# Kernel optimization log

Measured on AMD Instinct MI355X. Metric: run time of the kernel, lower is better.

## Reference

```python
import jax, jax.numpy as jnp
import numpy as np

B, T, C, H, W = 16, 5, 512, 16, 16
NUM_FEAT = 10
K_IN = T * H * W          # 1280, conv1/G3 in_channels
G_OUT = NUM_FEAT * H * W  # 2560, G3 out_channels


def setup_inputs() -> dict:
    key = jax.random.key(0)
    ks = jax.random.split(key, 9)
    inp = {
        "input": jax.random.normal(ks[0], (B, T, C, H, W), dtype=jnp.float32),
        "input1": jax.random.normal(ks[1], (B, T, C, H, W), dtype=jnp.float32),
        "act_weights": jax.random.uniform(ks[2], (3,), dtype=jnp.float32),
        # Conv1d kernels with kernel_size=1 stored as [out_ch, in_ch]
        "conv1_w": jax.random.normal(ks[3], (NUM_FEAT, K_IN), dtype=jnp.float32) / np.sqrt(K_IN),
        "conv1_b": jax.random.normal(ks[4], (NUM_FEAT,), dtype=jnp.float32) * 0.01,
        "G3_w": jax.random.normal(ks[5], (G_OUT, K_IN), dtype=jnp.float32) / np.sqrt(K_IN),
        "G3_b": jax.random.normal(ks[6], (G_OUT,), dtype=jnp.float32) * 0.01,
        "ffnn1_w": jax.random.normal(ks[7], (C, C), dtype=jnp.float32) / np.sqrt(C),
        "ffnn1_b": jax.random.normal(ks[8], (C,), dtype=jnp.float32) * 0.01,
    }
    return inp


def reference(input, input1, act_weights, conv1_w, conv1_b, G3_w, G3_b, ffnn1_w, ffnn1_b):
    b, t, c, h, w = input.shape
    nf = conv1_w.shape[0]
    # [B,T,C,H,W] -> [B,C,T*H*W] -> transpose to [B, T*H*W, C] (conv1d channel axis = T*H*W)
    x = jnp.transpose(input, (0, 2, 1, 3, 4)).reshape(b, c, t * h * w)
    x = jnp.swapaxes(x, 1, 2)  # [B, K_IN, C]

    # conv1 (1x1 conv == GEMM over channel axis): [B, nf, C]
    c1 = jnp.einsum("fk,bkc->bfc", conv1_w, x) + conv1_b[None, :, None]
    # transpose -> [B, C, nf]; AvgPool1d(nf) -> mean over nf -> [B, C]
    pooled = jnp.mean(jnp.swapaxes(c1, 1, 2), axis=-1)
    # shared linear (same ffnn1 used in all three branches)
    pre = pooled @ ffnn1_w.T + ffnn1_b  # [B, C]

    # G3: [B, G_OUT, C] -> permute -> [B, C, G_OUT]
    g3 = jnp.einsum("gk,bkc->bgc", G3_w, x) + G3_b[None, :, None]
    g3 = jnp.swapaxes(g3, 1, 2)  # [B, C, G_OUT]

    # diag_embed(v) @ M == v[..., None] * M  -> fuse the three branches into one scale
    scale = (act_weights[0] * jax.nn.relu(pre)
             + act_weights[1] * jax.nn.sigmoid(pre)
             + act_weights[2] * jax.nn.softmax(pre, axis=1))  # [B, C]

    out = scale[:, :, None] * g3  # [B, C, nf*H*W]
    out = out.reshape(b, c, nf, h, w)
    return jnp.transpose(out, (0, 2, 1, 3, 4))  # [B, nf, C, H, W]
```

## Files before the change

### kernel.cpp

```cpp
#include <hip/hip_runtime.h>
#include <hip/hip_bf16.h>
#include <stdint.h>

#define B_   16
#define T_   5
#define C_   512
#define HW_  256
#define NF_  10
#define KIN_ 1280
#define GOUT_ 2560

typedef __attribute__((ext_vector_type(8))) short s16x8;
typedef __attribute__((ext_vector_type(4))) float f32x4;
typedef unsigned short u16;

__device__ __forceinline__ u16 f2bf(float x) {
    unsigned int u = __float_as_uint(x);
    return (u16)((u + 0x7FFFu + ((u >> 16) & 1u)) >> 16);
}

#define CASTW_N8  (GOUT_ * KIN_ / 8)
#define CASTW_BLKS (CASTW_N8 / 256)

__global__ __launch_bounds__(256) void k_init(const float* __restrict__ conv1_w,
                        const float* __restrict__ conv1_b,
                        float* __restrict__ wbar, float* __restrict__ bbar,
                        const float* __restrict__ g3w,
                        u16* __restrict__ wsA) {
    if (blockIdx.x < 5) {
        int k = blockIdx.x * 256 + threadIdx.x;
        float s = 0.f;
        #pragma unroll
        for (int f = 0; f < NF_; ++f) s += conv1_w[f * KIN_ + k];
        wbar[k] = s * (1.0f / NF_);
        if (blockIdx.x == 0 && threadIdx.x == 0) {
            float sb = 0.f;
            #pragma unroll
            for (int f = 0; f < NF_; ++f) sb += conv1_b[f];
            *bbar = sb * (1.0f / NF_);
        }
        return;
    }
    int i = (blockIdx.x - 5) * 256 + threadIdx.x;
    if (i < CASTW_N8) {
        const float4* s = reinterpret_cast<const float4*>(g3w) + (size_t)i * 2;
        float4 v0 = s[0], v1 = s[1];
        union { u16 h[8]; int4 v; } u;
        u.h[0] = f2bf(v0.x); u.h[1] = f2bf(v0.y); u.h[2] = f2bf(v0.z); u.h[3] = f2bf(v0.w);
        u.h[4] = f2bf(v1.x); u.h[5] = f2bf(v1.y); u.h[6] = f2bf(v1.z); u.h[7] = f2bf(v1.w);
        reinterpret_cast<int4*>(wsA)[i] = u.v;
    }
}

__global__ void k_wbar(const float* __restrict__ conv1_w,
                       const float* __restrict__ conv1_b,
                       float* __restrict__ wbar, float* __restrict__ bbar) {
    int k = blockIdx.x * blockDim.x + threadIdx.x;
    if (k < KIN_) {
        float s = 0.f;
        #pragma unroll
        for (int f = 0; f < NF_; ++f) s += conv1_w[f * KIN_ + k];
        wbar[k] = s * (1.0f / NF_);
    }
    if (blockIdx.x == 0 && threadIdx.x == 0) {
        float s = 0.f;
        #pragma unroll
        for (int f = 0; f < NF_; ++f) s += conv1_b[f];
        *bbar = s * (1.0f / NF_);
    }
}

#define FUSE_BLKS (B_ * C_)

__global__ __launch_bounds__(256) void k_prep(const float* __restrict__ in,
                         const float* __restrict__ wbar,
                         const float* __restrict__ bbar,
                         float* __restrict__ pooled,
                         u16* __restrict__ X) {
    int bc = blockIdx.x;
    int b = bc >> 9;
    int c = bc & 511;
    int tid = threadIdx.x;

    float s = 0.f;
    if (tid < 160) {
        int t   = tid >> 5;
        int hw0 = (tid & 31) * 8;
        size_t off = ((size_t)(b * T_ + t) * C_ + c) * HW_ + hw0;
        const float4* ip = reinterpret_cast<const float4*>(in + off);
        float4 v0 = ip[0], v1 = ip[1];
        const float4* wp = reinterpret_cast<const float4*>(wbar + t * HW_ + hw0);
        float4 w0 = wp[0], w1 = wp[1];
        s = v0.x * w0.x + v0.y * w0.y + v0.z * w0.z + v0.w * w0.w
          + v1.x * w1.x + v1.y * w1.y + v1.z * w1.z + v1.w * w1.w;
        union { u16 h[8]; int4 q; } u;
        u.h[0] = f2bf(v0.x); u.h[1] = f2bf(v0.y); u.h[2] = f2bf(v0.z); u.h[3] = f2bf(v0.w);
        u.h[4] = f2bf(v1.x); u.h[5] = f2bf(v1.y); u.h[6] = f2bf(v1.z); u.h[7] = f2bf(v1.w);
        reinterpret_cast<int4*>(X + off)[0] = u.q;
    }

    #pragma unroll
    for (int off = 32; off > 0; off >>= 1) s += __shfl_down(s, off, 64);
    __shared__ float red[4];
    int wid = tid >> 6, lane = tid & 63;
    if (lane == 0) red[wid] = s;
    __syncthreads();
    if (tid == 0) {
        float tot = red[0] + red[1] + red[2] + red[3];
        pooled[bc] = tot + *bbar;
    }
}

__global__ __launch_bounds__(256) void k_pooled(const float* __restrict__ in,
                         const float* __restrict__ wbar,
                         const float* __restrict__ bbar,
                         float* __restrict__ pooled) {
    int bc = blockIdx.x;
    int b = bc >> 9;
    int c = bc & 511;
    int hw = threadIdx.x;
    const float* base = in + ((size_t)(b * T_) * C_ + c) * HW_;
    float s = 0.f;
    #pragma unroll
    for (int t = 0; t < T_; ++t)
        s = fmaf(wbar[t * HW_ + hw], base[(size_t)t * C_ * HW_ + hw], s);
    #pragma unroll
    for (int off = 32; off > 0; off >>= 1) s += __shfl_down(s, off, 64);
    __shared__ float red[4];
    int wid = threadIdx.x >> 6, lane = threadIdx.x & 63;
    if (lane == 0) red[wid] = s;
    __syncthreads();
    if (threadIdx.x == 0) {
        float tot = red[0] + red[1] + red[2] + red[3];
        pooled[bc] = tot + *bbar;
    }
}

__global__ __launch_bounds__(256) void k_pre(const float* __restrict__ pooled,
                       const float* __restrict__ ffnn1_w,
                       const float* __restrict__ ffnn1_b,
                       float* __restrict__ pre) {
    int b   = blockIdx.x >> 4;
    int grp = blockIdx.x & 15;
    int wid = threadIdx.x >> 6, lane = threadIdx.x & 63;

    const float4* pp = reinterpret_cast<const float4*>(pooled + b * C_ + lane * 8);
    float4 pa = pp[0], pb = pp[1];

    #pragma unroll
    for (int rr = 0; rr < 8; ++rr) {
        int c = grp * 32 + wid * 8 + rr;
        const float4* wr = reinterpret_cast<const float4*>(ffnn1_w + (size_t)c * C_ + lane * 8);
        float4 wa = wr[0], wb2 = wr[1];
        float d = pa.x * wa.x + pa.y * wa.y + pa.z * wa.z + pa.w * wa.w
                + pb.x * wb2.x + pb.y * wb2.y + pb.z * wb2.z + pb.w * wb2.w;
        #pragma unroll
        for (int off = 32; off > 0; off >>= 1) d += __shfl_xor(d, off, 64);
        if (lane == 0) pre[b * C_ + c] = d + ffnn1_b[c];
    }
}

__global__ __launch_bounds__(512) void k_act(const float* __restrict__ pre,
                       const float* __restrict__ actw,
                       float* __restrict__ scale) {
    int b = blockIdx.x;
    int tid = threadIdx.x;
    int wid = tid >> 6, lane = tid & 63;
    __shared__ float redm[8], reds[8];

    float p0 = pre[b * C_ + tid];
    float mx = p0;
    #pragma unroll
    for (int off = 32; off > 0; off >>= 1) mx = fmaxf(mx, __shfl_xor(mx, off, 64));
    if (lane == 0) redm[wid] = mx;
    __syncthreads();
    float m8 = redm[0];
    #pragma unroll
    for (int i = 1; i < 8; ++i) m8 = fmaxf(m8, redm[i]);
    float e0 = __expf(p0 - m8);
    float sm = e0;
    #pragma unroll
    for (int off = 32; off > 0; off >>= 1) sm += __shfl_xor(sm, off, 64);
    if (lane == 0) reds[wid] = sm;
    __syncthreads();
    float ssum = reds[0];
    #pragma unroll
    for (int i = 1; i < 8; ++i) ssum += reds[i];

    float aw0 = actw[0], aw1 = actw[1], aw2 = actw[2];
    scale[b * C_ + tid] = aw0 * fmaxf(p0, 0.f)
                        + aw1 * (1.f / (1.f + __expf(-p0)))
                        + aw2 * (e0 / ssum);
}

__global__ __launch_bounds__(512) void k_scale(const float* __restrict__ pooled,
                        const float* __restrict__ ffnn1_w,
                        const float* __restrict__ ffnn1_b,
                        const float* __restrict__ actw,
                        float* __restrict__ scale) {
    int b = blockIdx.x;
    int c = threadIdx.x;
    __shared__ float sp[C_];
    __shared__ float red[8];

    sp[c] = pooled[b * C_ + c];
    __syncthreads();

    float acc = ffnn1_b[c];
    const float* wr = ffnn1_w + (size_t)c * C_;
    #pragma unroll 8
    for (int j = 0; j < C_; ++j) acc = fmaf(wr[j], sp[j], acc);

    int wid = c >> 6, lane = c & 63;
    float m = acc;
    #pragma unroll
    for (int off = 32; off > 0; off >>= 1) m = fmaxf(m, __shfl_down(m, off, 64));
    if (lane == 0) red[wid] = m;
    __syncthreads();
    if (c == 0) {
        float mm = red[0];
        #pragma unroll
        for (int i = 1; i < 8; ++i) mm = fmaxf(mm, red[i]);
        red[0] = mm;
    }
    __syncthreads();
    m = red[0];
    __syncthreads();

    float e = __expf(acc - m);
    float s = e;
    #pragma unroll
    for (int off = 32; off > 0; off >>= 1) s += __shfl_down(s, off, 64);
    if (lane == 0) red[wid] = s;
    __syncthreads();
    if (c == 0) {
        float ss = 0.f;
        #pragma unroll
        for (int i = 0; i < 8; ++i) ss += red[i];
        red[0] = ss;
    }
    __syncthreads();
    s = red[0];

    float w0 = actw[0], w1 = actw[1], w2 = actw[2];
    float val = w0 * fmaxf(acc, 0.f)
              + w1 * (1.f / (1.f + __expf(-acc)))
              + w2 * (e / s);
    scale[b * C_ + c] = val;
}

#define BM 160
#define BN 256
#define BK 32
#define NKT (KIN_ / BK)
#define ABUF (BM * BK)
#define BBUF (BN * BK)
#define BUFU (ABUF + BBUF)

__device__ __forceinline__ void gload16(const void* g, void* l) {
    __builtin_amdgcn_global_load_lds(
        (const __attribute__((address_space(1))) void*)g,
        (__attribute__((address_space(3))) void*)l, 16, 0, 0);
}

__global__ __launch_bounds__(256, 2) void k_gemm_mfma(
    const u16* __restrict__ A,
    const u16* __restrict__ X,
    const float* __restrict__ g3b,
    const float* __restrict__ scale,
    float* __restrict__ out)
{
    __shared__ u16 lds[2 * BUFU];

    int orig = blockIdx.x;
    int xcd  = orig & 7;
    int idx  = orig >> 3;
    int nt   = xcd * 4 + (idx >> 4);
    int gt   = idx & 15;
    int g0   = gt * BM;
    int b    = nt >> 1;
    int c0   = (nt & 1) * BN;

    int tid = threadIdx.x;
    int lane = tid & 63, wid = tid >> 6;
    int lrow = lane & 15, lslot = lane >> 4;

    int offA0, offA1, offA2, offB0, offB1, offB2, offB3;
    {
        int q, r, p;
        q = tid;        r = q >> 2; p = q & 3; offA0 = r * KIN_ + (p ^ ((r >> 1) & 3)) * 8;
        q = 256 + tid;  r = q >> 2; p = q & 3; offA1 = r * KIN_ + (p ^ ((r >> 1) & 3)) * 8;
        q = 512 + tid;  r = q >> 2; p = q & 3; offA2 = r * KIN_ + (p ^ ((r >> 1) & 3)) * 8;
        q = tid;        r = q >> 2; p = q & 3; offB0 = r * HW_  + (p ^ ((r >> 1) & 3)) * 8;
        q = 256 + tid;  r = q >> 2; p = q & 3; offB1 = r * HW_  + (p ^ ((r >> 1) & 3)) * 8;
        q = 512 + tid;  r = q >> 2; p = q & 3; offB2 = r * HW_  + (p ^ ((r >> 1) & 3)) * 8;
        q = 768 + tid;  r = q >> 2; p = q & 3; offB3 = r * HW_  + (p ^ ((r >> 1) & 3)) * 8;
    }
    int wb = wid * 512;

    const u16* Abase = A + (size_t)g0 * KIN_;
    #define XOFF(kt) ((((size_t)(b * T_ + ((kt) >> 3)) * C_) + c0) * HW_ + ((kt) & 7) * 32)

    #define STAGE(D, sA, sX)                                                 \
    {                                                                        \
        gload16((sA) + offA0, (D) + wb);                                     \
        gload16((sA) + offA1, (D) + 2048 + wb);                              \
        if (tid < 128) gload16((sA) + offA2, (D) + 4096 + wb);               \
        gload16((sX) + offB0, (D) + ABUF + wb);                              \
        gload16((sX) + offB1, (D) + ABUF + 2048 + wb);                       \
        gload16((sX) + offB2, (D) + ABUF + 4096 + wb);                       \
        gload16((sX) + offB3, (D) + ABUF + 6144 + wb);                       \
    }

    STAGE(lds, Abase, X + XOFF(0));
    __syncthreads();

    f32x4 acc[10][4];
    #pragma unroll
    for (int m = 0; m < 10; ++m)
        #pragma unroll
        for (int n = 0; n < 4; ++n) acc[m][n] = (f32x4)0.f;

    int cur = 0;
    for (int t = 0; t < NKT; ++t) {
        const u16* Ac = lds + cur * BUFU;
        const u16* Bc = Ac + ABUF;
        if (t + 1 < NKT) {
            u16* Dn = lds + (cur ^ 1) * BUFU;
            const u16* sA = Abase + (size_t)(t + 1) * BK;
            const u16* sX = X + XOFF(t + 1);
            STAGE(Dn, sA, sX);
        }

        s16x8 b0[4];
        #pragma unroll
        for (int n = 0; n < 4; ++n) {
            int r = wid * 64 + n * 16 + lrow;
            int p = lslot ^ ((r >> 1) & 3);
            b0[n] = *reinterpret_cast<const s16x8*>(Bc + r * BK + p * 8);
        }
        __builtin_amdgcn_s_setprio(1);
        #pragma unroll
        for (int m = 0; m < 10; ++m) {
            int r = m * 16 + lrow;
            int p = lslot ^ ((r >> 1) & 3);
            s16x8 am = *reinterpret_cast<const s16x8*>(Ac + r * BK + p * 8);
            #pragma unroll
            for (int n = 0; n < 4; ++n)
                acc[m][n] = __builtin_amdgcn_mfma_f32_16x16x32_bf16(
                                am, b0[n], acc[m][n], 0, 0, 0);
        }
        __builtin_amdgcn_s_setprio(0);

        __syncthreads();
        cur ^= 1;
    }

    int cb = c0 + wid * 64;
    #pragma unroll
    for (int n = 0; n < 4; ++n) {
        int c = cb + n * 16 + lrow;
        float sc = scale[b * C_ + c];
        #pragma unroll
        for (int m = 0; m < 10; ++m) {
            int g  = g0 + m * 16 + lslot * 4;
            int f  = g >> 8;
            int hw = g & 255;
            float4 bias = *reinterpret_cast<const float4*>(g3b + g);
            f32x4 v = acc[m][n];
            float4 o;
            o.x = sc * (v[0] + bias.x);
            o.y = sc * (v[1] + bias.y);
            o.z = sc * (v[2] + bias.z);
            o.w = sc * (v[3] + bias.w);
            *reinterpret_cast<float4*>(
                out + (((size_t)(b * NF_ + f) * C_ + c) * HW_ + hw)) = o;
        }
    }
    #undef XOFF
    #undef STAGE
}

#define FBM 128
#define FBN 128
#define FBK 32
__global__ __launch_bounds__(256) void k_gemm_fp32(
    const float* __restrict__ in,
    const float* __restrict__ g3w,
    const float* __restrict__ g3b,
    const float* __restrict__ scale,
    float* __restrict__ out)
{
    int b  = blockIdx.y;
    int gt = blockIdx.x >> 2;
    int ct = blockIdx.x & 3;
    int g0 = gt * FBM, c0 = ct * FBN;
    int tid = threadIdx.x;
    int ty = tid & 15;
    int tx = tid >> 4;

    __shared__ float As[FBK][FBM + 4];
    __shared__ float Bs[FBK][FBN + 4];

    float acc[8][8];
    #pragma unroll
    for (int i = 0; i < 8; ++i)
        #pragma unroll
        for (int j = 0; j < 8; ++j) acc[i][j] = 0.f;

    for (int k0 = 0; k0 < KIN_; k0 += FBK) {
        int t   = k0 >> 8;
        int hw0 = k0 & 255;
        #pragma unroll
        for (int p = 0; p < 16; ++p) {
            int idx = tid + p * 256;
            int kk = idx & 31, gg = idx >> 5;
            As[kk][gg] = g3w[(size_t)(g0 + gg) * KIN_ + k0 + kk];
        }
        const float* bsrc = in + ((size_t)(b * T_ + t) * C_ + c0) * HW_ + hw0;
        #pragma unroll
        for (int p = 0; p < 16; ++p) {
            int idx = tid + p * 256;
            int kk = idx & 31, cc = idx >> 5;
            Bs[kk][cc] = bsrc[(size_t)cc * HW_ + kk];
        }
        __syncthreads();
        #pragma unroll
        for (int kk = 0; kk < FBK; ++kk) {
            float a[8], bb[8];
            #pragma unroll
            for (int i = 0; i < 8; ++i) a[i] = As[kk][ty * 8 + i];
            #pragma unroll
            for (int j = 0; j < 8; ++j) bb[j] = Bs[kk][tx * 8 + j];
            #pragma unroll
            for (int i = 0; i < 8; ++i)
                #pragma unroll
                for (int j = 0; j < 8; ++j)
                    acc[i][j] = fmaf(a[i], bb[j], acc[i][j]);
        }
        __syncthreads();
    }

    int gl = ty * 8;
    int g  = g0 + gl;
    int f  = g >> 8;
    int hw = g & 255;
    #pragma unroll
    for (int j = 0; j < 8; ++j) {
        int c = c0 + tx * 8 + j;
        float sc = scale[b * C_ + c];
        float* op = out + (((size_t)(b * NF_ + f) * C_ + c) * HW_ + hw);
        float4 v0, v1;
        v0.x = sc * (acc[0][j] + g3b[g + 0]);
        v0.y = sc * (acc[1][j] + g3b[g + 1]);
        v0.z = sc * (acc[2][j] + g3b[g + 2]);
        v0.w = sc * (acc[3][j] + g3b[g + 3]);
        v1.x = sc * (acc[4][j] + g3b[g + 4]);
        v1.y = sc * (acc[5][j] + g3b[g + 5]);
        v1.z = sc * (acc[6][j] + g3b[g + 6]);
        v1.w = sc * (acc[7][j] + g3b[g + 7]);
        reinterpret_cast<float4*>(op)[0] = v0;
        reinterpret_cast<float4*>(op)[1] = v1;
    }
}

extern "C" void kernel_launch(void* const* d_in, const int* in_sizes, int n_in,
                              void* d_out, int out_size, void* d_ws, size_t ws_size,
                              hipStream_t stream) {
    const float* input    = (const float*)d_in[0];
    const float* actw     = (const float*)d_in[2];
    const float* conv1_w  = (const float*)d_in[3];
    const float* conv1_b  = (const float*)d_in[4];
    const float* g3w      = (const float*)d_in[5];
    const float* g3b      = (const float*)d_in[6];
    const float* ffnn1_w  = (const float*)d_in[7];
    const float* ffnn1_b  = (const float*)d_in[8];
    float* out = (float*)d_out;

    float* ws     = (float*)d_ws;
    float* wbar   = ws;
    float* bbar   = ws + KIN_;
    float* pooled = ws + 1536;
    float* pre    = ws + 1536 + B_ * C_;
    float* scale  = pooled;
    u16* wsA = (u16*)(ws + 17920);
    u16* wsX = wsA + (size_t)GOUT_ * KIN_;
    const size_t need = 71680ull + (size_t)GOUT_ * KIN_ * 2 + (size_t)B_ * T_ * C_ * HW_ * 2;

    if (ws_size >= need) {
        k_init<<<dim3(5 + CASTW_BLKS), dim3(256), 0, stream>>>(
            conv1_w, conv1_b, wbar, bbar, g3w, wsA);
        k_prep<<<dim3(FUSE_BLKS), dim3(256), 0, stream>>>(
            input, wbar, bbar, pooled, wsX);
        k_pre<<<dim3(256), dim3(256), 0, stream>>>(pooled, ffnn1_w, ffnn1_b, pre);
        k_act<<<dim3(B_), dim3(512), 0, stream>>>(pre, actw, scale);
        k_gemm_mfma<<<dim3(512), dim3(256), 0, stream>>>(
            wsA, wsX, g3b, scale, out);
    } else {
        k_wbar<<<dim3((KIN_ + 255) / 256), dim3(256), 0, stream>>>(conv1_w, conv1_b, wbar, bbar);
        k_pooled<<<dim3(B_ * C_), dim3(256), 0, stream>>>(input, wbar, bbar, pooled);
        k_scale<<<dim3(B_), dim3(512), 0, stream>>>(pooled, ffnn1_w, ffnn1_b, actw, pre);
        k_gemm_fp32<<<dim3((GOUT_ / FBM) * (C_ / FBN), B_), dim3(256), 0, stream>>>(
            input, g3w, g3b, pre, out);
    }
}
```

Before: 88.09 us.

## Retile MFMA GEMM to 160x128 with BK=64 and 2x2 warp grid

Changes the G3 GEMM tile from 160x256 with BK=32 to 160x128 with BK=64. K is now split into two 32-wide LDS planes per stage, and the four warps are arranged 2x2 over M and N instead of 1x4 along N. The grid doubles to 1024 blocks to improve occupancy and load balance across the CUs, and each stage now issues half as many barriers per K. The cost is lower operand reuse per block, since each A tile is loaded twice as often, plus a larger LDS footprint per buffer.

```diff
diff --git a/kernel.cpp b/kernel.cpp
--- a/kernel.cpp
+++ b/kernel.cpp
@@ -250,12 +250,13 @@
 }
 
 #define BM 160
-#define BN 256
-#define BK 32
+#define BN 128
+#define BK 64
 #define NKT (KIN_ / BK)
-#define ABUF (BM * BK)
-#define BBUF (BN * BK)
-#define BUFU (ABUF + BBUF)
+#define APL 5120
+#define BPL 4096
+#define ABUFU (2 * APL)
+#define BUFU (ABUFU + 2 * BPL)
 
 __device__ __forceinline__ void gload16(const void* g, void* l) {
     __builtin_amdgcn_global_load_lds(
@@ -275,95 +276,127 @@
     int orig = blockIdx.x;
     int xcd  = orig & 7;
     int idx  = orig >> 3;
-    int nt   = xcd * 4 + (idx >> 4);
+    int nt   = xcd * 8 + (idx >> 4);
     int gt   = idx & 15;
     int g0   = gt * BM;
-    int b    = nt >> 1;
-    int c0   = (nt & 1) * BN;
+    int b    = nt >> 2;
+    int c0   = (nt & 3) * BN;
 
     int tid = threadIdx.x;
     int lane = tid & 63, wid = tid >> 6;
+    int wr = wid >> 1, wc = wid & 1;
     int lrow = lane & 15, lslot = lane >> 4;
 
-    int offA0, offA1, offA2, offB0, offB1, offB2, offB3;
-    {
-        int q, r, p;
-        q = tid;        r = q >> 2; p = q & 3; offA0 = r * KIN_ + (p ^ ((r >> 1) & 3)) * 8;
-        q = 256 + tid;  r = q >> 2; p = q & 3; offA1 = r * KIN_ + (p ^ ((r >> 1) & 3)) * 8;
-        q = 512 + tid;  r = q >> 2; p = q & 3; offA2 = r * KIN_ + (p ^ ((r >> 1) & 3)) * 8;
-        q = tid;        r = q >> 2; p = q & 3; offB0 = r * HW_  + (p ^ ((r >> 1) & 3)) * 8;
-        q = 256 + tid;  r = q >> 2; p = q & 3; offB1 = r * HW_  + (p ^ ((r >> 1) & 3)) * 8;
-        q = 512 + tid;  r = q >> 2; p = q & 3; offB2 = r * HW_  + (p ^ ((r >> 1) & 3)) * 8;
-        q = 768 + tid;  r = q >> 2; p = q & 3; offB3 = r * HW_  + (p ^ ((r >> 1) & 3)) * 8;
+    int offA[5], offB[4];
+    #pragma unroll
+    for (int i = 0; i < 5; ++i) {
+        int q = i * 256 + tid;
+        int pl = (q >= 640) ? 1 : 0;
+        int rem = q - pl * 640;
+        int r = rem >> 2, ps = rem & 3;
+        int s = ps ^ ((r >> 1) & 3);
+        offA[i] = r * KIN_ + pl * 32 + s * 8;
+    }
+    #pragma unroll
+    for (int i = 0; i < 4; ++i) {
+        int q = i * 256 + tid;
+        int pl = q >> 9;
+        int rem = q & 511;
+        int r = rem >> 2, ps = rem & 3;
+        int s = ps ^ ((r >> 1) & 3);
+        offB[i] = r * HW_ + pl * 32 + s * 8;
     }
     int wb = wid * 512;
 
     const u16* Abase = A + (size_t)g0 * KIN_;
-    #define XOFF(kt) ((((size_t)(b * T_ + ((kt) >> 3)) * C_) + c0) * HW_ + ((kt) & 7) * 32)
+    #define XOFF(kt) ((((size_t)(b * T_ + ((kt) >> 2)) * C_) + c0) * HW_ + ((kt) & 3) * 64)
 
     #define STAGE(D, sA, sX)                                                 \
     {                                                                        \
-        gload16((sA) + offA0, (D) + wb);                                     \
-        gload16((sA) + offA1, (D) + 2048 + wb);                              \
-        if (tid < 128) gload16((sA) + offA2, (D) + 4096 + wb);               \
-        gload16((sX) + offB0, (D) + ABUF + wb);                              \
-        gload16((sX) + offB1, (D) + ABUF + 2048 + wb);                       \
-        gload16((sX) + offB2, (D) + ABUF + 4096 + wb);                       \
-        gload16((sX) + offB3, (D) + ABUF + 6144 + wb);                       \
+        gload16((sA) + offA[0], (D) + wb);                                   \
+        gload16((sA) + offA[1], (D) + 2048 + wb);                            \
+        gload16((sA) + offA[2], (D) + 4096 + wb);                            \
+        gload16((sA) + offA[3], (D) + 6144 + wb);                            \
+        gload16((sA) + offA[4], (D) + 8192 + wb);                            \
+        gload16((sX) + offB[0], (D) + ABUFU + wb);                           \
+        gload16((sX) + offB[1], (D) + ABUFU + 2048 + wb);                    \
+        gload16((sX) + offB[2], (D) + ABUFU + 4096 + wb);                    \
+        gload16((sX) + offB[3], (D) + ABUFU + 6144 + wb);                    \
     }
 
     STAGE(lds, Abase, X + XOFF(0));
     __syncthreads();
 
-    f32x4 acc[10][4];
-    #pragma unroll
-    for (int m = 0; m < 10; ++m)
+    f32x4 acc[5][4];
+    #pragma unroll
+    for (int m = 0; m < 5; ++m)
         #pragma unroll
         for (int n = 0; n < 4; ++n) acc[m][n] = (f32x4)0.f;
 
     int cur = 0;
     for (int t = 0; t < NKT; ++t) {
         const u16* Ac = lds + cur * BUFU;
-        const u16* Bc = Ac + ABUF;
+        const u16* Bc = Ac + ABUFU;
         if (t + 1 < NKT) {
             u16* Dn = lds + (cur ^ 1) * BUFU;
-            const u16* sA = Abase + (size_t)(t + 1) * BK;
-            const u16* sX = X + XOFF(t + 1);
-            STAGE(Dn, sA, sX);
-        }
-
-        s16x8 b0[4];
+            STAGE(Dn, Abase + (size_t)(t + 1) * BK, X + XOFF(t + 1));
+        }
+
+        s16x8 b0[4], a0[5];
         #pragma unroll
         for (int n = 0; n < 4; ++n) {
-            int r = wid * 64 + n * 16 + lrow;
+            int r = wc * 64 + n * 16 + lrow;
             int p = lslot ^ ((r >> 1) & 3);
-            b0[n] = *reinterpret_cast<const s16x8*>(Bc + r * BK + p * 8);
+            b0[n] = *reinterpret_cast<const s16x8*>(Bc + r * 32 + p * 8);
+        }
+        #pragma unroll
+        for (int m = 0; m < 5; ++m) {
+            int r = wr * 80 + m * 16 + lrow;
+            int p = lslot ^ ((r >> 1) & 3);
+            a0[m] = *reinterpret_cast<const s16x8*>(Ac + r * 32 + p * 8);
         }
         __builtin_amdgcn_s_setprio(1);
         #pragma unroll
-        for (int m = 0; m < 10; ++m) {
-            int r = m * 16 + lrow;
-            int p = lslot ^ ((r >> 1) & 3);
-            s16x8 am = *reinterpret_cast<const s16x8*>(Ac + r * BK + p * 8);
+        for (int m = 0; m < 5; ++m)
             #pragma unroll
             for (int n = 0; n < 4; ++n)
                 acc[m][n] = __builtin_amdgcn_mfma_f32_16x16x32_bf16(
-                                am, b0[n], acc[m][n], 0, 0, 0);
-        }
+                                a0[m], b0[n], acc[m][n], 0, 0, 0);
+        __builtin_amdgcn_s_setprio(0);
+
+        s16x8 b1[4], a1[5];
+        #pragma unroll
+        for (int n = 0; n < 4; ++n) {
+            int r = wc * 64 + n * 16 + lrow;
+            int p = lslot ^ ((r >> 1) & 3);
+            b1[n] = *reinterpret_cast<const s16x8*>(Bc + BPL + r * 32 + p * 8);
+        }
+        #pragma unroll
+        for (int m = 0; m < 5; ++m) {
+            int r = wr * 80 + m * 16 + lrow;
+            int p = lslot ^ ((r >> 1) & 3);
+            a1[m] = *reinterpret_cast<const s16x8*>(Ac + APL + r * 32 + p * 8);
+        }
+        __builtin_amdgcn_s_setprio(1);
+        #pragma unroll
+        for (int m = 0; m < 5; ++m)
+            #pragma unroll
+            for (int n = 0; n < 4; ++n)
+                acc[m][n] = __builtin_amdgcn_mfma_f32_16x16x32_bf16(
+                                a1[m], b1[n], acc[m][n], 0, 0, 0);
         __builtin_amdgcn_s_setprio(0);
 
         __syncthreads();
         cur ^= 1;
     }
 
-    int cb = c0 + wid * 64;
     #pragma unroll
     for (int n = 0; n < 4; ++n) {
-        int c = cb + n * 16 + lrow;
+        int c = c0 + wc * 64 + n * 16 + lrow;
         float sc = scale[b * C_ + c];
         #pragma unroll
-        for (int m = 0; m < 10; ++m) {
-            int g  = g0 + m * 16 + lslot * 4;
+        for (int m = 0; m < 5; ++m) {
+            int g  = g0 + wr * 80 + m * 16 + lslot * 4;
             int f  = g >> 8;
             int hw = g & 255;
             float4 bias = *reinterpret_cast<const float4*>(g3b + g);
@@ -494,7 +527,7 @@
             input, wbar, bbar, pooled, wsX);
         k_pre<<<dim3(256), dim3(256), 0, stream>>>(pooled, ffnn1_w, ffnn1_b, pre);
         k_act<<<dim3(B_), dim3(512), 0, stream>>>(pre, actw, scale);
-        k_gemm_mfma<<<dim3(512), dim3(256), 0, stream>>>(
+        k_gemm_mfma<<<dim3(1024), dim3(256), 0, stream>>>(
             wsA, wsX, g3b, scale, out);
     } else {
         k_wbar<<<dim3((KIN_ + 255) / 256), dim3(256), 0, stream>>>(conv1_w, conv1_b, wbar, bbar);
```

Measured after the change: 91.57 us. 1.04x slower.
